# Performance work log

Measured on AMD Instinct MI355X. Metric: run time of the kernel, lower is better.

The kernel has to match this reference:

```python
import jax, jax.numpy as jnp
import numpy as np

SPARSITY = 0.1
B, N, K = 256, 65536, 64

def setup_inputs() -> dict:
    key = jax.random.key(0)
    kx, kc = jax.random.split(key)
    x = jax.random.normal(kx, (B, N), dtype=jnp.float32)
    cluster_assignments = jax.random.randint(kc, (N,), 0, K, dtype=jnp.int32)
    cluster_weights = jnp.ones((K,), dtype=jnp.float32)
    return {"x": x, "cluster_weights": cluster_weights, "cluster_assignments": cluster_assignments}

def reference(x, cluster_weights, cluster_assignments):
    b, n = x.shape
    k = cluster_weights.shape[0]
    # cluster activation prob (context=None path): softmax(weights), same for all batch rows
    p = jax.nn.softmax(cluster_weights) * SPARSITY                      # [K]
    ku, kv = jax.random.split(jax.random.key(42))
    u = jax.random.uniform(ku, (b, n))   # drives the random permutation per (batch, cluster)
    v = jax.random.uniform(kv, (b, n))   # drives the binomial count (sum of Bernoullis)
    # Binomial(len(cluster_i), p_i) == sum of per-neuron Bernoulli(p_i) over the cluster
    bern = (v < p[cluster_assignments][None, :]).astype(jnp.int32)      # [B, N]
    counts = jax.vmap(lambda row: jax.ops.segment_sum(row, cluster_assignments, num_segments=k))(bern)  # [B, K]
    counts = jnp.maximum(counts, 1)                                     # max(1, binomial sample)
    # within-cluster uniform-random ranking: sort by (cluster, u); rank = pos - cluster_start
    sizes = jnp.bincount(cluster_assignments, length=k)                 # [K]
    starts = jnp.cumsum(sizes) - sizes                                  # exclusive cumsum [K]
    cluster_sorted = jnp.sort(cluster_assignments)                      # [N], batch-independent
    pos_in_cluster = jnp.arange(n) - starts[cluster_sorted]             # [N]
    keys = cluster_assignments.astype(jnp.float32)[None, :] + u * 0.999  # cluster-major composite key
    order = jnp.argsort(keys, axis=1)                                   # [B, N]
    mask_sorted = (pos_in_cluster[None, :] < counts[:, cluster_sorted]).astype(x.dtype)  # [B, N]
    mask = jnp.zeros_like(x).at[jnp.arange(b)[:, None], order].set(mask_sorted)
    return x * mask
```

## Files before the change

kernel.cpp:

```cpp
#include <hip/hip_runtime.h>
#include <stdint.h>

#define NROWS 256
#define NCOLS 65536
#define KCL   64
#define TMAX  20
#define NBLK  128
#define CHUNK (NCOLS / NBLK)

__device__ __forceinline__ void tf2x32(uint32_t k0, uint32_t k1,
                                       uint32_t x0, uint32_t x1,
                                       uint32_t& o0, uint32_t& o1) {
  const uint32_t ks2 = k0 ^ k1 ^ 0x1BD11BDAu;
  x0 += k0; x1 += k1;
#define TFR(r) { x0 += x1; x1 = (x1 << (r)) | (x1 >> (32 - (r))); x1 ^= x0; }
  TFR(13) TFR(15) TFR(26) TFR(6)
  x0 += k1; x1 += ks2 + 1u;
  TFR(17) TFR(29) TFR(16) TFR(24)
  x0 += ks2; x1 += k0 + 2u;
  TFR(13) TFR(15) TFR(26) TFR(6)
  x0 += k0; x1 += k1 + 3u;
  TFR(17) TFR(29) TFR(16) TFR(24)
  x0 += k1; x1 += ks2 + 4u;
  TFR(13) TFR(15) TFR(26) TFR(6)
  x0 += ks2; x1 += k0 + 5u;
#undef TFR
  o0 = x0; o1 = x1;
}

__device__ __forceinline__ uint32_t jax_bits(uint32_t k0, uint32_t k1, uint32_t f) {
  uint32_t o0, o1;
  tf2x32(k0, k1, 0u, f, o0, o1);
  return o0 ^ o1;
}

__device__ __forceinline__ float bits_to_u01(uint32_t bits) {
  return __uint_as_float((bits >> 9) | 0x3f800000u) - 1.0f;
}

__device__ __forceinline__ float key_from_ubits(uint32_t ubits, float kf) {
  return __fadd_rn(kf, __fmul_rn(bits_to_u01(ubits), 0.999f));
}

__device__ __forceinline__ int wave_sum_i(int v) {
#pragma unroll
  for (int m = 1; m < 64; m <<= 1) v += __shfl_xor(v, m, 64);
  return v;
}
__device__ __forceinline__ uint32_t wave_min_u(uint32_t v) {
#pragma unroll
  for (int m = 1; m < 64; m <<= 1) {
    const uint32_t o = (uint32_t)__shfl_xor((int)v, m, 64);
    v = (o < v) ? o : v;
  }
  return v;
}
__device__ __forceinline__ int wave_min_i(int v) {
#pragma unroll
  for (int m = 1; m < 64; m <<= 1) {
    const int o = __shfl_xor(v, m, 64);
    v = (o < v) ? o : v;
  }
  return v;
}

__global__ __launch_bounds__(256)
void k_hist(const int* __restrict__ a, int* __restrict__ blockhist) {
  __shared__ int h[KCL];
  const int tid = threadIdx.x;
  if (tid < KCL) h[tid] = 0;
  __syncthreads();
  const int base = blockIdx.x * CHUNK;
#pragma unroll
  for (int i = base + tid; i < base + CHUNK; i += 256)
    atomicAdd(&h[a[i]], 1);
  __syncthreads();
  if (tid < KCL) blockhist[blockIdx.x * KCL + tid] = h[tid];
}

__global__ void k_prefix_setup(int* __restrict__ blockhist, int* __restrict__ sizes,
                               int* __restrict__ starts,
                               const float* __restrict__ w, uint32_t* __restrict__ hdr,
                               float* __restrict__ p) {
  const int k = threadIdx.x;
  if (k < KCL) {
    int acc = 0;
#pragma unroll 8
    for (int blk = 0; blk < NBLK; ++blk) {
      const int t = blockhist[blk * KCL + k];
      blockhist[blk * KCL + k] = acc;
      acc += t;
    }
    sizes[k] = acc;
  }
  __syncthreads();
  if (k == 0) {
    int acc = 0;
    for (int i = 0; i < KCL; ++i) { starts[i] = acc; acc += sizes[i]; }
    uint32_t o0, o1;
    tf2x32(0u, 42u, 0u, 0u, o0, o1); hdr[0] = o0; hdr[1] = o1;
    tf2x32(0u, 42u, 0u, 1u, o0, o1); hdr[2] = o0; hdr[3] = o1;
    float m = -3.402823466e38f;
    for (int i = 0; i < KCL; ++i) m = fmaxf(m, w[i]);
    float s = 0.0f;
    for (int i = 0; i < KCL; ++i) s += expf(w[i] - m);
    for (int i = 0; i < KCL; ++i) p[i] = (expf(w[i] - m) / s) * 0.1f;
  }
}

__global__ __launch_bounds__(256)
void k_scatter(const int* __restrict__ a, const int* __restrict__ blockhist,
               const int* __restrict__ starts, int* __restrict__ idx_sorted) {
  __shared__ int cur[KCL];
  const int tid = threadIdx.x;
  if (tid < KCL) cur[tid] = starts[tid] + blockhist[blockIdx.x * KCL + tid];
  __syncthreads();
  const int base = blockIdx.x * CHUNK;
#pragma unroll
  for (int i = base + tid; i < base + CHUNK; i += 256) {
    const int k = a[i];
    const int slot = atomicAdd(&cur[k], 1);
    idx_sorted[slot] = i;
  }
}

__global__ __launch_bounds__(256)
void k_select(const float* __restrict__ x,
              const int* __restrict__ idx_sorted,
              const int* __restrict__ sizes,
              const int* __restrict__ starts,
              const uint32_t* __restrict__ hdr,
              const float* __restrict__ p,
              float* __restrict__ out) {
  const int lane = threadIdx.x & 63;
  const int pair = (blockIdx.x << 2) + (threadIdx.x >> 6);
  const int b = pair & (NROWS - 1);
  const int k = pair >> 8;

  int sz = sizes[k];
  const int st = starts[k];
  if (sz <= 0) return;
  if (sz > TMAX * 64) sz = TMAX * 64;

  const uint32_t ku0 = hdr[0], ku1 = hdr[1], kv0 = hdr[2], kv1 = hdr[3];
  const float pk = p[k];
  const float kf = (float)k;

  uint32_t kb[TMAX];
  int cnt = 0;
#pragma unroll
  for (int t = 0; t < TMAX; ++t) {
    const int j = lane + (t << 6);
    uint32_t kbv = 0xFFFFFFFFu;
    if (j < sz) {
      const int n = idx_sorted[st + j];
      const uint32_t f = (uint32_t)((b << 16) + n);
      const uint32_t ubv = jax_bits(ku0, ku1, f);
      const uint32_t vbv = jax_bits(kv0, kv1, f);
      cnt += (bits_to_u01(vbv) < pk) ? 1 : 0;
      kbv = __float_as_uint(key_from_ubits(ubv, kf));
    }
    kb[t] = kbv;
  }
  int C = wave_sum_i(cnt);
  if (C < 1) C = 1;

  uint32_t consumed = 0;
  uint32_t Tkey;
  for (int e = 0;; ++e) {
    uint32_t mn = 0xFFFFFFFFu;
#pragma unroll
    for (int t = 0; t < TMAX; ++t)
      if (!(consumed & (1u << t)) && kb[t] < mn) mn = kb[t];
    const uint32_t wmn = wave_min_u(mn);
    if (e == C - 1) { Tkey = wmn; break; }
    const unsigned long long bal = __ballot(mn == wmn);
    const int src = (int)__ffsll((long long)bal) - 1;
    if (lane == src) {
      bool done = false;
#pragma unroll
      for (int t = 0; t < TMAX; ++t) {
        if (!done && !(consumed & (1u << t)) && kb[t] == wmn) {
          consumed |= (1u << t); done = true;
        }
      }
    }
  }

  int below = 0, tloc = 0;
#pragma unroll
  for (int t = 0; t < TMAX; ++t) {
    below += (kb[t] < Tkey) ? 1 : 0;
    tloc  += (kb[t] == Tkey) ? 1 : 0;
  }
  const int nbelow = wave_sum_i(below);
  const int tieCnt = wave_sum_i(tloc);
  const int r = C - nbelow;

  int cutN = 0x7FFFFFFF;
  if (r < tieCnt) {
    uint32_t cons2 = 0;
    for (int e = 0; e < r; ++e) {
      int mnN = 0x7FFFFFFF, mnT = 0;
#pragma unroll
      for (int t = 0; t < TMAX; ++t) {
        if (kb[t] == Tkey && !(cons2 & (1u << t))) {
          const int n = idx_sorted[st + lane + (t << 6)];
          if (n < mnN) { mnN = n; mnT = t; }
        }
      }
      const int w = wave_min_i(mnN);
      cutN = w;
      const unsigned long long bal = __ballot(mnN == w);
      const int src = (int)__ffsll((long long)bal) - 1;
      if (lane == src) cons2 |= (1u << mnT);
    }
  }

  const size_t rowoff = (size_t)b * NCOLS;
#pragma unroll
  for (int t = 0; t < TMAX; ++t) {
    const uint32_t v = kb[t];
    bool sel = (v < Tkey);
    if (!sel && v == Tkey) {
      if (r >= tieCnt) {
        sel = true;
      } else {
        const int n = idx_sorted[st + lane + (t << 6)];
        sel = (n <= cutN);
      }
    }
    if (sel) {
      const int n = idx_sorted[st + lane + (t << 6)];
      const size_t off = rowoff + (uint32_t)n;
      out[off] = x[off];
    }
  }
}

extern "C" void kernel_launch(void* const* d_in, const int* in_sizes, int n_in,
                              void* d_out, int out_size, void* d_ws, size_t ws_size,
                              hipStream_t stream) {
  const float* x = (const float*)d_in[0];
  const float* w = (const float*)d_in[1];
  const int* assign = (const int*)d_in[2];
  float* out = (float*)d_out;
  uint32_t* ws = (uint32_t*)d_ws;

  uint32_t* hdr       = ws;
  float*    p         = (float*)(ws + 4);
  int*      sizes     = (int*)(ws + 68);
  int*      starts    = (int*)(ws + 132);
  int*      blockhist = (int*)(ws + 196);
  int*      idxs      = (int*)(ws + 196 + NBLK * KCL);

  hipMemsetAsync(d_out, 0, (size_t)out_size * sizeof(float), stream);

  k_hist<<<NBLK, 256, 0, stream>>>(assign, blockhist);
  k_prefix_setup<<<1, 64, 0, stream>>>(blockhist, sizes, starts, w, hdr, p);
  k_scatter<<<NBLK, 256, 0, stream>>>(assign, blockhist, starts, idxs);
  k_select<<<(NROWS * KCL) / 4, 256, 0, stream>>>(x, idxs, sizes, starts, hdr, p, out);
  (void)n_in; (void)in_sizes; (void)ws_size;
}
```

Measured before the change: 118.9 us.

## Fuse output zeroing into histogram kernel and streamline per-wave selection loop

Replaces the separate memset with a zeroing pass folded into the histogram kernel, which now runs 2048 blocks with 128 of them also building histograms. Prefix setup uses wave shuffles for the cluster scan and softmax and precomputes an integer Bernoulli threshold, so the select kernel compares raw bits instead of converting them to floats. The selection loop keeps a per-lane running minimum, updated only by the lane that consumed the element, instead of rescanning all registers every iteration. It also preloads indices and packs two reductions into one. The risks are extra register pressure and slight rounding differences from the integer threshold.

Measured after the change: 105.3 us. 11.5% less time.

```diff
diff --git a/kernel.cpp b/kernel.cpp
--- a/kernel.cpp
+++ b/kernel.cpp
@@ -7,6 +7,7 @@
 #define TMAX  20
 #define NBLK  128
 #define CHUNK (NCOLS / NBLK)
+#define ZBLK  2048
 
 __device__ __forceinline__ void tf2x32(uint32_t k0, uint32_t k1,
                                        uint32_t x0, uint32_t x1,
@@ -65,46 +66,60 @@
 }
 
 __global__ __launch_bounds__(256)
-void k_hist(const int* __restrict__ a, int* __restrict__ blockhist) {
-  __shared__ int h[KCL];
-  const int tid = threadIdx.x;
-  if (tid < KCL) h[tid] = 0;
-  __syncthreads();
-  const int base = blockIdx.x * CHUNK;
-#pragma unroll
-  for (int i = base + tid; i < base + CHUNK; i += 256)
-    atomicAdd(&h[a[i]], 1);
-  __syncthreads();
-  if (tid < KCL) blockhist[blockIdx.x * KCL + tid] = h[tid];
+void k_zerohist(float4* __restrict__ outv, const int* __restrict__ a,
+                int* __restrict__ blockhist) {
+  const int gtid = blockIdx.x * 256 + threadIdx.x;
+  const float4 z = make_float4(0.f, 0.f, 0.f, 0.f);
+#pragma unroll
+  for (int i = 0; i < 8; ++i)
+    outv[gtid + i * (ZBLK * 256)] = z;
+  if (blockIdx.x < NBLK) {
+    __shared__ int h[KCL];
+    if (threadIdx.x < KCL) h[threadIdx.x] = 0;
+    __syncthreads();
+    const int base = blockIdx.x * CHUNK;
+#pragma unroll
+    for (int i = base + threadIdx.x; i < base + CHUNK; i += 256)
+      atomicAdd(&h[a[i]], 1);
+    __syncthreads();
+    if (threadIdx.x < KCL) blockhist[blockIdx.x * KCL + threadIdx.x] = h[threadIdx.x];
+  }
 }
 
 __global__ void k_prefix_setup(int* __restrict__ blockhist, int* __restrict__ sizes,
                                int* __restrict__ starts,
                                const float* __restrict__ w, uint32_t* __restrict__ hdr,
-                               float* __restrict__ p) {
+                               uint32_t* __restrict__ vthresh) {
   const int k = threadIdx.x;
-  if (k < KCL) {
-    int acc = 0;
+  int acc = 0;
 #pragma unroll 8
-    for (int blk = 0; blk < NBLK; ++blk) {
-      const int t = blockhist[blk * KCL + k];
-      blockhist[blk * KCL + k] = acc;
-      acc += t;
-    }
-    sizes[k] = acc;
-  }
-  __syncthreads();
+  for (int blk = 0; blk < NBLK; ++blk) {
+    const int t = blockhist[blk * KCL + k];
+    blockhist[blk * KCL + k] = acc;
+    acc += t;
+  }
+  sizes[k] = acc;
+  int scan = acc;
+#pragma unroll
+  for (int d = 1; d < 64; d <<= 1) {
+    const int o = __shfl_up(scan, d, 64);
+    if (k >= d) scan += o;
+  }
+  starts[k] = scan - acc;
+  const float wk = w[k];
+  float m = wk;
+#pragma unroll
+  for (int d = 1; d < 64; d <<= 1) m = fmaxf(m, __shfl_xor(m, d, 64));
+  const float e = expf(wk - m);
+  float s = e;
+#pragma unroll
+  for (int d = 1; d < 64; d <<= 1) s += __shfl_xor(s, d, 64);
+  const float pk = (e / s) * 0.1f;
+  vthresh[k] = (uint32_t)ceilf(pk * 8388608.0f);
   if (k == 0) {
-    int acc = 0;
-    for (int i = 0; i < KCL; ++i) { starts[i] = acc; acc += sizes[i]; }
     uint32_t o0, o1;
     tf2x32(0u, 42u, 0u, 0u, o0, o1); hdr[0] = o0; hdr[1] = o1;
     tf2x32(0u, 42u, 0u, 1u, o0, o1); hdr[2] = o0; hdr[3] = o1;
-    float m = -3.402823466e38f;
-    for (int i = 0; i < KCL; ++i) m = fmaxf(m, w[i]);
-    float s = 0.0f;
-    for (int i = 0; i < KCL; ++i) s += expf(w[i] - m);
-    for (int i = 0; i < KCL; ++i) p[i] = (expf(w[i] - m) / s) * 0.1f;
   }
 }
 
@@ -130,7 +145,7 @@
               const int* __restrict__ sizes,
               const int* __restrict__ starts,
               const uint32_t* __restrict__ hdr,
-              const float* __restrict__ p,
+              const uint32_t* __restrict__ vthresh,
               float* __restrict__ out) {
   const int lane = threadIdx.x & 63;
   const int pair = (blockIdx.x << 2) + (threadIdx.x >> 6);
@@ -143,24 +158,33 @@
   if (sz > TMAX * 64) sz = TMAX * 64;
 
   const uint32_t ku0 = hdr[0], ku1 = hdr[1], kv0 = hdr[2], kv1 = hdr[3];
-  const float pk = p[k];
+  const uint32_t vt = vthresh[k];
   const float kf = (float)k;
+  const uint32_t bbase = (uint32_t)(b << 16);
+
+  int nv[TMAX];
+#pragma unroll
+  for (int t = 0; t < TMAX; ++t) {
+    const int j = lane + (t << 6);
+    nv[t] = (j < sz) ? idx_sorted[st + j] : 0;
+  }
 
   uint32_t kb[TMAX];
+  uint32_t curmin = 0xFFFFFFFFu;
   int cnt = 0;
 #pragma unroll
   for (int t = 0; t < TMAX; ++t) {
     const int j = lane + (t << 6);
     uint32_t kbv = 0xFFFFFFFFu;
     if (j < sz) {
-      const int n = idx_sorted[st + j];
-      const uint32_t f = (uint32_t)((b << 16) + n);
+      const uint32_t f = bbase + (uint32_t)nv[t];
       const uint32_t ubv = jax_bits(ku0, ku1, f);
       const uint32_t vbv = jax_bits(kv0, kv1, f);
-      cnt += (bits_to_u01(vbv) < pk) ? 1 : 0;
+      cnt += ((vbv >> 9) < vt) ? 1 : 0;
       kbv = __float_as_uint(key_from_ubits(ubv, kf));
     }
     kb[t] = kbv;
+    curmin = (kbv < curmin) ? kbv : curmin;
   }
   int C = wave_sum_i(cnt);
   if (C < 1) C = 1;
@@ -168,33 +192,35 @@
   uint32_t consumed = 0;
   uint32_t Tkey;
   for (int e = 0;; ++e) {
-    uint32_t mn = 0xFFFFFFFFu;
-#pragma unroll
-    for (int t = 0; t < TMAX; ++t)
-      if (!(consumed & (1u << t)) && kb[t] < mn) mn = kb[t];
-    const uint32_t wmn = wave_min_u(mn);
+    const uint32_t wmn = wave_min_u(curmin);
     if (e == C - 1) { Tkey = wmn; break; }
-    const unsigned long long bal = __ballot(mn == wmn);
+    const unsigned long long bal = __ballot(curmin == wmn);
     const int src = (int)__ffsll((long long)bal) - 1;
     if (lane == src) {
-      bool done = false;
+      int ct = -1;
+#pragma unroll
+      for (int t = 0; t < TMAX; ++t)
+        if (ct < 0 && !((consumed >> t) & 1u) && kb[t] == wmn) ct = t;
+      consumed |= (1u << ct);
+      uint32_t nm = 0xFFFFFFFFu;
 #pragma unroll
       for (int t = 0; t < TMAX; ++t) {
-        if (!done && !(consumed & (1u << t)) && kb[t] == wmn) {
-          consumed |= (1u << t); done = true;
-        }
+        const uint32_t v = ((consumed >> t) & 1u) ? 0xFFFFFFFFu : kb[t];
+        nm = (v < nm) ? v : nm;
       }
-    }
-  }
-
-  int below = 0, tloc = 0;
-#pragma unroll
-  for (int t = 0; t < TMAX; ++t) {
-    below += (kb[t] < Tkey) ? 1 : 0;
-    tloc  += (kb[t] == Tkey) ? 1 : 0;
-  }
-  const int nbelow = wave_sum_i(below);
-  const int tieCnt = wave_sum_i(tloc);
+      curmin = nm;
+    }
+  }
+
+  int packed = 0;
+#pragma unroll
+  for (int t = 0; t < TMAX; ++t) {
+    packed += (kb[t] < Tkey) ? (1 << 16) : 0;
+    packed += (kb[t] == Tkey) ? 1 : 0;
+  }
+  const int sred = wave_sum_i(packed);
+  const int nbelow = sred >> 16;
+  const int tieCnt = sred & 0xFFFF;
   const int r = C - nbelow;
 
   int cutN = 0x7FFFFFFF;
@@ -248,17 +274,15 @@
   uint32_t* ws = (uint32_t*)d_ws;
 
   uint32_t* hdr       = ws;
-  float*    p         = (float*)(ws + 4);
+  uint32_t* vthresh   = ws + 4;
   int*      sizes     = (int*)(ws + 68);
   int*      starts    = (int*)(ws + 132);
   int*      blockhist = (int*)(ws + 196);
   int*      idxs      = (int*)(ws + 196 + NBLK * KCL);
 
-  hipMemsetAsync(d_out, 0, (size_t)out_size * sizeof(float), stream);
-
-  k_hist<<<NBLK, 256, 0, stream>>>(assign, blockhist);
-  k_prefix_setup<<<1, 64, 0, stream>>>(blockhist, sizes, starts, w, hdr, p);
+  k_zerohist<<<ZBLK, 256, 0, stream>>>((float4*)out, assign, blockhist);
+  k_prefix_setup<<<1, 64, 0, stream>>>(blockhist, sizes, starts, w, hdr, vthresh);
   k_scatter<<<NBLK, 256, 0, stream>>>(assign, blockhist, starts, idxs);
-  k_select<<<(NROWS * KCL) / 4, 256, 0, stream>>>(x, idxs, sizes, starts, hdr, p, out);
+  k_select<<<(NROWS * KCL) / 4, 256, 0, stream>>>(x, idxs, sizes, starts, hdr, vthresh, out);
   (void)n_in; (void)in_sizes; (void)ws_size;
 }
```
